# Kernel optimization log

Measured on AMD Instinct MI355X. Metric: run time of the kernel, lower is better.

Reference implementation:

```python
import jax, jax.numpy as jnp
import numpy as np

INPUT_DIM, PROJ_DIM, HIDDEN = 1, 16, 32
B, T = 2048, 2048


def setup_inputs() -> dict:
    key = jax.random.key(0)
    ks = jax.random.split(key, 9)
    s_in = 1.0 / np.sqrt(INPUT_DIM)
    s_h = 1.0 / np.sqrt(HIDDEN)
    s_p = 1.0 / np.sqrt(PROJ_DIM)
    return {
        "x_seq": jax.random.normal(ks[0], (B, T, INPUT_DIM), dtype=jnp.float32),
        # input_linear: Linear(input_dim, proj_dim)
        "Wp": jax.random.uniform(ks[1], (PROJ_DIM, INPUT_DIM), minval=-s_in, maxval=s_in),
        "bp": jax.random.uniform(ks[2], (PROJ_DIM,), minval=-s_in, maxval=s_in),
        # LSTM weights (PyTorch gate order i,f,g,o)
        "W_ih": jax.random.uniform(ks[3], (4 * HIDDEN, PROJ_DIM), minval=-s_h, maxval=s_h),
        "W_hh": jax.random.uniform(ks[4], (4 * HIDDEN, HIDDEN), minval=-s_h, maxval=s_h),
        "b_ih": jax.random.uniform(ks[5], (4 * HIDDEN,), minval=-s_h, maxval=s_h),
        "b_hh": jax.random.uniform(ks[6], (4 * HIDDEN,), minval=-s_h, maxval=s_h),
        # output_linear: Linear(hidden, input_dim)
        "Wo": jax.random.uniform(ks[7], (INPUT_DIM, HIDDEN), minval=-s_h, maxval=s_h),
        "bo": jax.random.uniform(ks[8], (INPUT_DIM,), minval=-s_h, maxval=s_h),
    }


def reference(x_seq, Wp, bp, W_ih, W_hh, b_ih, b_hh, Wo, bo):
    H = W_hh.shape[1]
    b, t, _ = x_seq.shape
    # input projection for all timesteps at once (same math as per-step Linear)
    # then pre-apply W_ih: [B,T,4H]
    xp = jnp.einsum("bti,pi->btp", x_seq, Wp) + bp
    gates_x = jnp.einsum("btp,gp->btg", xp, W_ih) + b_ih + b_hh
    gates_x = jnp.transpose(gates_x, (1, 0, 2))  # [T,B,4H]

    def step(carry, gx):
        h, c = carry
        gates = gx + h @ W_hh.T  # [B,4H]
        i, f, g, o = jnp.split(gates, 4, axis=-1)
        i = jax.nn.sigmoid(i)
        f = jax.nn.sigmoid(f)
        g = jnp.tanh(g)
        o = jax.nn.sigmoid(o)
        c = f * c + i * g
        h = o * jnp.tanh(c)
        return (h, c), h

    h0 = jnp.zeros((b, H), dtype=x_seq.dtype)
    c0 = jnp.zeros((b, H), dtype=x_seq.dtype)
    (_, _), hs = jax.lax.scan(step, (h0, c0), gates_x)  # hs: [T,B,H]
    outputs = jnp.einsum("tbh,oh->bto", hs, Wo) + bo  # [B,T,input_dim]
    return outputs
```

## Files before the change

kernel.cpp:

```cpp
#include <hip/hip_runtime.h>


#define BB 2048
#define TT 2048
#define HH 32

typedef _Float16 h2 __attribute__((ext_vector_type(2)));

__device__ __forceinline__ float gate_eval(float x, float m, float a, float b) {
    float e = __builtin_amdgcn_exp2f(x * m);
    float r = __builtin_amdgcn_rcpf(1.0f + e);
    return fmaf(a, r, b);
}

template <int CTRL>
__device__ __forceinline__ int dpp_mov(int v) {
    return __builtin_amdgcn_update_dpp(0, v, CTRL, 0xf, 0xf, true);
}

template <int CTRL>
__device__ __forceinline__ float dpp_add(float v) {
    int s = __builtin_amdgcn_update_dpp(0, __float_as_int(v), CTRL, 0xf, 0xf, true);
    return v + __int_as_float(s);
}

struct HVec { int v[16]; };

__device__ __forceinline__ HVec gather_net(float h) {
    _Float16 hf = (_Float16)h;
    unsigned hb = (unsigned)__builtin_bit_cast(unsigned short, hf);
    int dup = (int)(hb | (hb << 16));
    int prt = __builtin_amdgcn_ds_swizzle(dup, 0x401F);
    HVec r;
    r.v[0] = (int)__builtin_amdgcn_perm((unsigned)prt, (unsigned)dup, 0x07060100u);
    r.v[1] = dpp_mov<0xB1>(r.v[0]);
    r.v[2] = dpp_mov<0x4E>(r.v[0]);
    r.v[3] = dpp_mov<0x4E>(r.v[1]);
    r.v[4] = dpp_mov<0x124>(r.v[0]);
    r.v[5] = dpp_mov<0x124>(r.v[1]);
    r.v[6] = dpp_mov<0x124>(r.v[2]);
    r.v[7] = dpp_mov<0x124>(r.v[3]);
    r.v[8]  = dpp_mov<0x128>(r.v[0]);
    r.v[9]  = dpp_mov<0x128>(r.v[1]);
    r.v[10] = dpp_mov<0x128>(r.v[2]);
    r.v[11] = dpp_mov<0x128>(r.v[3]);
    r.v[12] = dpp_mov<0x128>(r.v[4]);
    r.v[13] = dpp_mov<0x128>(r.v[5]);
    r.v[14] = dpp_mov<0x128>(r.v[6]);
    r.v[15] = dpp_mov<0x128>(r.v[7]);
    return r;
}

__global__ __launch_bounds__(256) void lstm_fused_kernel(
    const float* __restrict__ x_seq,
    const float* __restrict__ Wp,
    const float* __restrict__ bp,
    const float* __restrict__ W_ih,
    const float* __restrict__ W_hh,
    const float* __restrict__ b_ih,
    const float* __restrict__ b_hh,
    const float* __restrict__ Wo,
    const float* __restrict__ bo,
    float* __restrict__ out)
{
    const int tid  = threadIdx.x;
    const int wave = tid >> 6;
    const int lane = tid & 63;
    const int half = lane >> 5;
    const int j    = lane & 31;
    const int b    = blockIdx.x * 8 + wave * 2 + half;

    const int rI = j, rF = HH + j, rG = 2 * HH + j, rO = 3 * HH + j;

    HVec idx = gather_net((float)j);
    h2 wI[16], wF[16], wG[16], wO[16];
    {
        const float* pI = W_hh + rI * HH;
        const float* pF = W_hh + rF * HH;
        const float* pG = W_hh + rG * HH;
        const float* pO = W_hh + rO * HH;
#pragma unroll
        for (int s = 0; s < 16; ++s) {
            h2 iv = __builtin_bit_cast(h2, idx.v[s]);
            int kx = (int)(float)iv.x;
            int ky = (int)(float)iv.y;
            wI[s].x = (_Float16)pI[kx]; wI[s].y = (_Float16)pI[ky];
            wF[s].x = (_Float16)pF[kx]; wF[s].y = (_Float16)pF[ky];
            wG[s].x = (_Float16)pG[kx]; wG[s].y = (_Float16)pG[ky];
            wO[s].x = (_Float16)pO[kx]; wO[s].y = (_Float16)pO[ky];
        }
    }

    float aI = 0.f, cI = 0.f, aF = 0.f, cF = 0.f;
    float aG = 0.f, cG = 0.f, aO = 0.f, cO = 0.f;
#pragma unroll
    for (int p = 0; p < 16; ++p) {
        float wpv = Wp[p], bpv = bp[p];
        float wi = W_ih[rI * 16 + p], wf = W_ih[rF * 16 + p];
        float wg = W_ih[rG * 16 + p], wo_ = W_ih[rO * 16 + p];
        aI = fmaf(wi, wpv, aI);  cI = fmaf(wi, bpv, cI);
        aF = fmaf(wf, wpv, aF);  cF = fmaf(wf, bpv, cF);
        aG = fmaf(wg, wpv, aG);  cG = fmaf(wg, bpv, cG);
        aO = fmaf(wo_, wpv, aO); cO = fmaf(wo_, bpv, cO);
    }
    cI += b_ih[rI] + b_hh[rI];
    cF += b_ih[rF] + b_hh[rF];
    cG += b_ih[rG] + b_hh[rG];
    cO += b_ih[rO] + b_hh[rO];

    const float LOG2E = 1.44269504088896340736f;
    const float woj = Wo[j];
    const float bo0 = bo[0];

    float c = 0.0f;
    const float* xp = x_seq + (size_t)b * TT;
    float* op = out + (size_t)b * TT;

    HVec hcur;
#pragma unroll
    for (int s = 0; s < 16; ++s) hcur.v[s] = 0;

    float4 x4 = *(const float4*)(xp);

    for (int t = 0; t < TT; t += 4) {
        const int tn = (t + 4 < TT) ? (t + 4) : t;
        float4 x4n = *(const float4*)(xp + tn);
        float outv[4];
#pragma unroll
        for (int u = 0; u < 4; ++u) {
            float xv = (u == 0) ? x4.x : (u == 1) ? x4.y : (u == 2) ? x4.z : x4.w;

            float sI0 = cI, sI1 = xv * aI;
            float sF0 = cF, sF1 = xv * aF;
            float sG0 = cG, sG1 = xv * aG;
            float sO0 = cO, sO1 = xv * aO;
#pragma unroll
            for (int k = 0; k < 16; k += 2) {
                h2 h0 = __builtin_bit_cast(h2, hcur.v[k]);
                h2 h1 = __builtin_bit_cast(h2, hcur.v[k + 1]);
                sI0 = __builtin_amdgcn_fdot2(wI[k],     h0, sI0, false);
                sF0 = __builtin_amdgcn_fdot2(wF[k],     h0, sF0, false);
                sG0 = __builtin_amdgcn_fdot2(wG[k],     h0, sG0, false);
                sO0 = __builtin_amdgcn_fdot2(wO[k],     h0, sO0, false);
                sI1 = __builtin_amdgcn_fdot2(wI[k + 1], h1, sI1, false);
                sF1 = __builtin_amdgcn_fdot2(wF[k + 1], h1, sF1, false);
                sG1 = __builtin_amdgcn_fdot2(wG[k + 1], h1, sG1, false);
                sO1 = __builtin_amdgcn_fdot2(wO[k + 1], h1, sO1, false);
            }

            float iv = gate_eval(sI0 + sI1, -LOG2E, 1.0f, 0.0f);
            float fv = gate_eval(sF0 + sF1, -LOG2E, 1.0f, 0.0f);
            float gv = gate_eval(sG0 + sG1, -2.0f * LOG2E, 2.0f, -1.0f);
            float ov = gate_eval(sO0 + sO1, -LOG2E, 1.0f, 0.0f);

            c = fmaf(fv, c, iv * gv);
            float th = gate_eval(c, -2.0f * LOG2E, 2.0f, -1.0f);
            float h = ov * th;

            hcur = gather_net(h);

            float po = woj * h;
            po = dpp_add<0x111>(po);
            po = dpp_add<0x112>(po);
            po = dpp_add<0x114>(po);
            po = dpp_add<0x118>(po);
            po = dpp_add<0x142>(po);
            outv[u] = po + bo0;
        }
        if ((lane & 31) == 31) {
            *(float4*)(op + t) = make_float4(outv[0], outv[1], outv[2], outv[3]);
        }
        x4 = x4n;
    }
}

extern "C" void kernel_launch(void* const* d_in, const int* in_sizes, int n_in,
                              void* d_out, int out_size, void* d_ws, size_t ws_size,
                              hipStream_t stream) {
    const float* x_seq = (const float*)d_in[0];
    const float* Wp    = (const float*)d_in[1];
    const float* bp    = (const float*)d_in[2];
    const float* W_ih  = (const float*)d_in[3];
    const float* W_hh  = (const float*)d_in[4];
    const float* b_ih  = (const float*)d_in[5];
    const float* b_hh  = (const float*)d_in[6];
    const float* Wo    = (const float*)d_in[7];
    const float* bo    = (const float*)d_in[8];
    float* out = (float*)d_out;

    dim3 grid(BB / 8);
    dim3 block(256);
    lstm_fused_kernel<<<grid, block, 0, stream>>>(
        x_seq, Wp, bp, W_ih, W_hh, b_ih, b_hh, Wo, bo, out);
}
```

Baseline: 731.0 us.

## Split LSTM gates across wave halves, one batch element per wave

Each wave now handles one batch element instead of two. Each 32-lane half evaluates two of the four gates (i/g or f/o), and the gate activations are exchanged with a cross-half shuffle. This halves the serial fdot2 chain per timestep and the weight registers per lane, and doubles the number of waves so the latency-bound recurrence can interleave better. In exchange it adds a cross-half shuffle on the critical path of every step, computes the cell update redundantly in both halves, and does somewhat more total instructions per batch element.

```diff
diff --git a/kernel.cpp b/kernel.cpp
--- a/kernel.cpp
+++ b/kernel.cpp
@@ -68,47 +68,42 @@
     const int lane = tid & 63;
     const int half = lane >> 5;
     const int j    = lane & 31;
-    const int b    = blockIdx.x * 8 + wave * 2 + half;
+    const int b    = blockIdx.x * 4 + wave;
 
-    const int rI = j, rF = HH + j, rG = 2 * HH + j, rO = 3 * HH + j;
+    const int r1 = half * HH + j;
+    const int r2 = 2 * HH + half * HH + j;
 
     HVec idx = gather_net((float)j);
-    h2 wI[16], wF[16], wG[16], wO[16];
+    h2 w1[16], w2[16];
     {
-        const float* pI = W_hh + rI * HH;
-        const float* pF = W_hh + rF * HH;
-        const float* pG = W_hh + rG * HH;
-        const float* pO = W_hh + rO * HH;
+        const float* p1 = W_hh + r1 * HH;
+        const float* p2 = W_hh + r2 * HH;
 #pragma unroll
         for (int s = 0; s < 16; ++s) {
             h2 iv = __builtin_bit_cast(h2, idx.v[s]);
             int kx = (int)(float)iv.x;
             int ky = (int)(float)iv.y;
-            wI[s].x = (_Float16)pI[kx]; wI[s].y = (_Float16)pI[ky];
-            wF[s].x = (_Float16)pF[kx]; wF[s].y = (_Float16)pF[ky];
-            wG[s].x = (_Float16)pG[kx]; wG[s].y = (_Float16)pG[ky];
-            wO[s].x = (_Float16)pO[kx]; wO[s].y = (_Float16)pO[ky];
+            w1[s].x = (_Float16)p1[kx]; w1[s].y = (_Float16)p1[ky];
+            w2[s].x = (_Float16)p2[kx]; w2[s].y = (_Float16)p2[ky];
         }
     }
 
-    float aI = 0.f, cI = 0.f, aF = 0.f, cF = 0.f;
-    float aG = 0.f, cG = 0.f, aO = 0.f, cO = 0.f;
+    float a1 = 0.f, c1 = 0.f, a2 = 0.f, c2 = 0.f;
 #pragma unroll
     for (int p = 0; p < 16; ++p) {
         float wpv = Wp[p], bpv = bp[p];
-        float wi = W_ih[rI * 16 + p], wf = W_ih[rF * 16 + p];
-        float wg = W_ih[rG * 16 + p], wo_ = W_ih[rO * 16 + p];
-        aI = fmaf(wi, wpv, aI);  cI = fmaf(wi, bpv, cI);
-        aF = fmaf(wf, wpv, aF);  cF = fmaf(wf, bpv, cF);
-        aG = fmaf(wg, wpv, aG);  cG = fmaf(wg, bpv, cG);
-        aO = fmaf(wo_, wpv, aO); cO = fmaf(wo_, bpv, cO);
+        float wi1 = W_ih[r1 * 16 + p], wi2 = W_ih[r2 * 16 + p];
+        a1 = fmaf(wi1, wpv, a1);  c1 = fmaf(wi1, bpv, c1);
+        a2 = fmaf(wi2, wpv, a2);  c2 = fmaf(wi2, bpv, c2);
     }
-    cI += b_ih[rI] + b_hh[rI];
-    cF += b_ih[rF] + b_hh[rF];
-    cG += b_ih[rG] + b_hh[rG];
-    cO += b_ih[rO] + b_hh[rO];
+    c1 += b_ih[r1] + b_hh[r1];
+    c2 += b_ih[r2] + b_hh[r2];
 
     const float LOG2E = 1.44269504088896340736f;
+    const float m2  = half ? -LOG2E : -2.0f * LOG2E;
+    const float a2c = half ? 1.0f : 2.0f;
+    const float b2c = half ? 0.0f : -1.0f;
+
     const float woj = Wo[j];
     const float bo0 = bo[0];
 
@@ -130,28 +125,27 @@
         for (int u = 0; u < 4; ++u) {
             float xv = (u == 0) ? x4.x : (u == 1) ? x4.y : (u == 2) ? x4.z : x4.w;
 
-            float sI0 = cI, sI1 = xv * aI;
-            float sF0 = cF, sF1 = xv * aF;
-            float sG0 = cG, sG1 = xv * aG;
-            float sO0 = cO, sO1 = xv * aO;
+            float s10 = c1, s11 = xv * a1;
+            float s20 = c2, s21 = xv * a2;
 #pragma unroll
             for (int k = 0; k < 16; k += 2) {
                 h2 h0 = __builtin_bit_cast(h2, hcur.v[k]);
                 h2 h1 = __builtin_bit_cast(h2, hcur.v[k + 1]);
-                sI0 = __builtin_amdgcn_fdot2(wI[k],     h0, sI0, false);
-                sF0 = __builtin_amdgcn_fdot2(wF[k],     h0, sF0, false);
-                sG0 = __builtin_amdgcn_fdot2(wG[k],     h0, sG0, false);
-                sO0 = __builtin_amdgcn_fdot2(wO[k],     h0, sO0, false);
-                sI1 = __builtin_amdgcn_fdot2(wI[k + 1], h1, sI1, false);
-                sF1 = __builtin_amdgcn_fdot2(wF[k + 1], h1, sF1, false);
-                sG1 = __builtin_amdgcn_fdot2(wG[k + 1], h1, sG1, false);
-                sO1 = __builtin_amdgcn_fdot2(wO[k + 1], h1, sO1, false);
+                s10 = __builtin_amdgcn_fdot2(w1[k],     h0, s10, false);
+                s20 = __builtin_amdgcn_fdot2(w2[k],     h0, s20, false);
+                s11 = __builtin_amdgcn_fdot2(w1[k + 1], h1, s11, false);
+                s21 = __builtin_amdgcn_fdot2(w2[k + 1], h1, s21, false);
             }
 
-            float iv = gate_eval(sI0 + sI1, -LOG2E, 1.0f, 0.0f);
-            float fv = gate_eval(sF0 + sF1, -LOG2E, 1.0f, 0.0f);
-            float gv = gate_eval(sG0 + sG1, -2.0f * LOG2E, 2.0f, -1.0f);
-            float ov = gate_eval(sO0 + sO1, -LOG2E, 1.0f, 0.0f);
+            float v1 = gate_eval(s10 + s11, -LOG2E, 1.0f, 0.0f);
+            float v2 = gate_eval(s20 + s21, m2, a2c, b2c);
+
+            float p1v = __shfl_xor(v1, 32, 64);
+            float p2v = __shfl_xor(v2, 32, 64);
+            float iv = half ? p1v : v1;
+            float fv = half ? v1 : p1v;
+            float gv = half ? p2v : v2;
+            float ov = half ? v2 : p2v;
 
             c = fmaf(fv, c, iv * gv);
             float th = gate_eval(c, -2.0f * LOG2E, 2.0f, -1.0f);
@@ -167,7 +161,7 @@
             po = dpp_add<0x142>(po);
             outv[u] = po + bo0;
         }
-        if ((lane & 31) == 31) {
+        if (lane == 63) {
             *(float4*)(op + t) = make_float4(outv[0], outv[1], outv[2], outv[3]);
         }
         x4 = x4n;
@@ -188,7 +182,7 @@
     const float* bo    = (const float*)d_in[8];
     float* out = (float*)d_out;
 
-    dim3 grid(BB / 8);
+    dim3 grid(BB / 4);
     dim3 block(256);
     lstm_fused_kernel<<<grid, block, 0, stream>>>(
         x_seq, Wp, bp, W_ih, W_hh, b_ih, b_hh, Wo, bo, out);
```

Result: slower. 875.9 us (+19.8%).
